# Optimization experiments

Hardware: AMD Instinct MI355X
Metric: run time of the kernel (lower is better)

## Reference

```python
import jax, jax.numpy as jnp
import numpy as np

B, D, C = 4096, 256, 10
KERNEL_MUL = 2.0
KERNEL_NUM = 5


def setup_inputs() -> dict:
    key = jax.random.key(0)
    k1, k2, k3, k4 = jax.random.split(key, 4)
    source = jax.random.normal(k1, (B, D), dtype=jnp.float32)
    target = jax.random.normal(k2, (B, D), dtype=jnp.float32)
    # source_label is consumed as a one-hot matrix by the module
    src_ids = jax.random.randint(k3, (B,), 0, C)
    source_label = jax.nn.one_hot(src_ids, C, dtype=jnp.float32)
    target_logits = jax.random.uniform(k4, (B, C), dtype=jnp.float32)
    return {"source": source, "target": target,
            "source_label": source_label, "target_logits": target_logits}


def _gaussian_kernel(x, y, kernel_mul, kernel_num):
    total = jnp.concatenate([x, y], axis=0)          # [n, d]
    n = total.shape[0]
    sq = jnp.sum(total * total, axis=1)               # [n]
    # ||a-b||^2 = ||a||^2 + ||b||^2 - 2 a.b  (same math, no [n,n,d] tensor)
    l2 = jnp.maximum(sq[:, None] + sq[None, :] - 2.0 * (total @ total.T), 0.0)
    n_f = jnp.asarray(n, l2.dtype)
    bandwidth = jnp.sum(l2) / (n_f * n_f - n_f)
    bandwidth = bandwidth / (kernel_mul ** (kernel_num // 2))
    kernels = jnp.zeros_like(l2)
    for i in range(kernel_num):
        kernels = kernels + jnp.exp(-l2 / (bandwidth * (kernel_mul ** i)))
    return kernels


def _cal_weight(source_label, target_logits, num_class):
    # normalize source one-hot per class column
    s_sum = jnp.sum(source_label, axis=0, keepdims=True)
    s_sum = jnp.where(s_sum == 0, 100.0, s_sum)
    s = source_label / s_sum                           # [Bs, C]
    # hard target labels for presence mask
    t_label = jnp.argmax(target_logits, axis=1)
    t_onehot = jax.nn.one_hot(t_label, num_class, dtype=target_logits.dtype)
    # normalize soft target logits per class column
    t_sum = jnp.sum(target_logits, axis=0, keepdims=True)
    t_sum = jnp.where(t_sum == 0, 100.0, t_sum)
    t = target_logits / t_sum                          # [Bt, C]
    # class is counted only if present in both domains
    mask = (jnp.sum(s, axis=0) > 0) & (jnp.sum(t_onehot, axis=0) > 0)  # [C]
    maskf = mask.astype(s.dtype)
    sm = s * maskf[None, :]
    tm = t * maskf[None, :]
    count = jnp.sum(maskf)
    weight_ss = sm @ sm.T
    weight_tt = tm @ tm.T
    weight_st = sm @ tm.T
    safe = jnp.where(count > 0, count, 1.0)
    weight_ss = jnp.where(count > 0, weight_ss / safe, 0.0)
    weight_tt = jnp.where(count > 0, weight_tt / safe, 0.0)
    weight_st = jnp.where(count > 0, weight_st / safe, 0.0)
    return weight_ss, weight_tt, weight_st


def reference(source, target, source_label, target_logits):
    num_class = target_logits.shape[1]
    bs = source.shape[0]
    w_ss, w_tt, w_st = _cal_weight(source_label, target_logits, num_class)
    kernels = _gaussian_kernel(source, target, KERNEL_MUL, KERNEL_NUM)
    SS = kernels[:bs, :bs]
    TT = kernels[bs:, bs:]
    ST = kernels[:bs, bs:]
    loss = (jnp.sum(w_ss * SS) + jnp.sum(w_tt * TT)
            - 2.0 * jnp.sum(w_st * ST))
    # eval mode: lambda schedule multiplier = 1.0
    return loss * 1.0
```

## Files before the change

kernel.cpp:

```cpp
#include <hip/hip_runtime.h>
#include <hip/hip_bf16.h>

#define N_TOTAL 8192
#define BROWS   4096
#define DDIM    256
#define NCLS    10
#define NB      64
#define NTRI    (NB*(NB+1)/2)

typedef __attribute__((ext_vector_type(8))) short bf16x8;
typedef __attribute__((ext_vector_type(4))) float f32x4;
typedef __attribute__((ext_vector_type(8))) unsigned short u16x8;

static constexpr size_t OFF_X    = 0;
static constexpr size_t OFF_SQ   = 0x400000;
static constexpr size_t OFF_XU   = 0x408000;
static constexpr size_t OFF_CP   = 0x488000;
static constexpr size_t OFF_CLS  = 0x498000;
static constexpr size_t OFF_PRES = 0x499000;
static constexpr size_t OFF_SC   = 0x49A000;
static constexpr size_t OFF_PART = 0x49B000;


__device__ __forceinline__ void gload_lds16(const void* g, void* l) {
    __builtin_amdgcn_global_load_lds((const __attribute__((address_space(1))) void*)g,
                                     (__attribute__((address_space(3))) void*)l, 16, 0, 0);
}

__global__ void k_prep(const float* __restrict__ src, const float* __restrict__ tgt,
                       unsigned short* __restrict__ X, float* __restrict__ sq) {
    int wid  = threadIdx.x >> 6;
    int lane = threadIdx.x & 63;
    int row  = blockIdx.x * 4 + wid;
    const float* p = (row < BROWS) ? (src + (size_t)row * DDIM)
                                   : (tgt + (size_t)(row - BROWS) * DDIM);
    f32x4 v = *reinterpret_cast<const f32x4*>(p + lane * 4);
    unsigned short h[4];
    float ssum = 0.f;
#pragma unroll
    for (int e = 0; e < 4; ++e) {
        unsigned bits = __float_as_uint(v[e]);
        unsigned r = (bits + 0x7FFFu + ((bits >> 16) & 1u)) >> 16;
        h[e] = (unsigned short)r;
        float f = __uint_as_float(r << 16);
        ssum += f * f;
    }
    ushort4 us; us.x = h[0]; us.y = h[1]; us.z = h[2]; us.w = h[3];
    *reinterpret_cast<ushort4*>(X + (size_t)row * DDIM + lane * 4) = us;
#pragma unroll
    for (int off = 32; off > 0; off >>= 1) ssum += __shfl_xor(ssum, off);
    if (lane == 0) sq[row] = ssum;
}

__global__ void k_aux(const unsigned short* __restrict__ X,
                      const float* __restrict__ label, const float* __restrict__ logits,
                      float* __restrict__ colpart, float* __restrict__ clspart,
                      unsigned* __restrict__ prespart) {
    __shared__ float shbuf[8][256];
    __shared__ float cbuf[256][NCLS];
    __shared__ unsigned pm[128];
    int t = threadIdx.x;
    if (blockIdx.x < 64) {
        int b  = blockIdx.x;
        int cg = t & 31;
        int rs = t >> 5;
        const unsigned short* base = X + (size_t)(b * 128 + rs) * DDIM + cg * 8;
        float a[8];
#pragma unroll
        for (int e = 0; e < 8; ++e) a[e] = 0.f;
        for (int i = 0; i < 16; ++i) {
            u16x8 v = *reinterpret_cast<const u16x8*>(base + (size_t)i * 8 * DDIM);
#pragma unroll
            for (int e = 0; e < 8; ++e) a[e] += __uint_as_float((unsigned)v[e] << 16);
        }
#pragma unroll
        for (int e = 0; e < 8; ++e) shbuf[rs][cg * 8 + e] = a[e];
        __syncthreads();
        float s = 0.f;
#pragma unroll
        for (int k = 0; k < 8; ++k) s += shbuf[k][t];
        colpart[b * DDIM + t] = s;
    } else {
        int b = blockIdx.x - 64;
        int r = b * 128 + (t & 127);
        if (t < 128) {
            const float* lr = label + (size_t)r * NCLS;
#pragma unroll
            for (int c = 0; c < NCLS; ++c) cbuf[t][c] = lr[c];
        } else {
            const float* gr = logits + (size_t)r * NCLS;
            float bv = -1e30f; int bc = 0;
#pragma unroll
            for (int c = 0; c < NCLS; ++c) {
                float v = gr[c];
                cbuf[t][c] = v;
                if (v > bv) { bv = v; bc = c; }
            }
            pm[t - 128] = 1u << bc;
        }
        __syncthreads();
        if (t < NCLS) {
            float a = 0.f;
            for (int i = 0; i < 128; ++i) a += cbuf[i][t];
            clspart[b * 20 + t] = a;
        } else if (t < 2 * NCLS) {
            float a = 0.f;
            for (int i = 128; i < 256; ++i) a += cbuf[i][t - NCLS];
            clspart[b * 20 + t] = a;
        }
        if (t == 0) {
            unsigned p = 0;
            for (int i = 0; i < 128; ++i) p |= pm[i];
            prespart[b] = p;
        }
    }
}

__global__ void k_stats(const float* __restrict__ sq, const float* __restrict__ colpart,
                        const float* __restrict__ clspart, const unsigned* __restrict__ prespart,
                        float* __restrict__ scal) {
    __shared__ double dred[256];
    __shared__ float  cfin[2 * NCLS];
    __shared__ unsigned presAll;
    int t = threadIdx.x;

    double cd = 0.0;
    for (int b = 0; b < 64; ++b) cd += (double)colpart[b * DDIM + t];
    dred[t] = cd * cd;
    __syncthreads();
    for (int s = 128; s > 0; s >>= 1) { if (t < s) dred[t] += dred[t + s]; __syncthreads(); }
    double S_cs = dred[0];
    __syncthreads();

    double ss = 0.0;
    for (int k = 0; k < 32; ++k) ss += (double)sq[t + 256 * k];
    dred[t] = ss;
    __syncthreads();
    for (int s = 128; s > 0; s >>= 1) { if (t < s) dred[t] += dred[t + s]; __syncthreads(); }
    double S_sq = dred[0];
    __syncthreads();

    if (t < 2 * NCLS) {
        float a = 0.f;
        for (int b = 0; b < 32; ++b) a += clspart[b * 20 + t];
        cfin[t] = a;
    }
    if (t == 0) {
        unsigned p = 0;
        for (int b = 0; b < 32; ++b) p |= prespart[b];
        presAll = p;
    }
    __syncthreads();

    if (t == 0) {
        double nf = (double)N_TOTAL;
        double sum_l2 = 2.0 * nf * S_sq - 2.0 * S_cs;
        if (sum_l2 < 0.0) sum_l2 = 0.0;
        double bw = sum_l2 / (nf * nf - nf) / 4.0;
        scal[0] = (float)(-1.0 / (16.0 * bw));
        int count = 0;
        for (int c = 0; c < NCLS; ++c) {
            float sv = cfin[c], tv = cfin[NCLS + c];
            bool m = (sv > 0.f) && ((presAll >> c) & 1u);
            count += m ? 1 : 0;
            float sdiv = (sv == 0.f) ? 100.f : sv;
            float tdiv = (tv == 0.f) ? 100.f : tv;
            scal[6  + c] = m ? (1.f / sdiv) : 0.f;
            scal[16 + c] = m ? (1.f / tdiv) : 0.f;
        }
        scal[5] = (float)(count > 0 ? count : 1);
    }
}

__global__ void k_build_xu(const float* __restrict__ label, const float* __restrict__ logits,
                           const float* __restrict__ scal, unsigned short* __restrict__ XU) {
    int r = blockIdx.x * blockDim.x + threadIdx.x;
    if (r >= N_TOTAL) return;
    float v[NCLS];
    if (r < BROWS) {
        const float* lr = label + (size_t)r * NCLS;
#pragma unroll
        for (int c = 0; c < NCLS; ++c) v[c] = lr[c] * scal[6 + c];
    } else {
        const float* gr = logits + (size_t)(r - BROWS) * NCLS;
#pragma unroll
        for (int c = 0; c < NCLS; ++c) v[c] = -gr[c] * scal[16 + c];
    }
    unsigned packed[16];
#pragma unroll
    for (int w = 0; w < 16; ++w) {
        unsigned lo = 0, hi = 0;
        if (2 * w < NCLS) {
            unsigned bits = __float_as_uint(v[2 * w]);
            lo = (bits + 0x7FFFu + ((bits >> 16) & 1u)) >> 16;
        }
        if (2 * w + 1 < NCLS) {
            unsigned bits = __float_as_uint(v[2 * w + 1]);
            hi = (bits + 0x7FFFu + ((bits >> 16) & 1u)) >> 16;
        }
        packed[w] = lo | (hi << 16);
    }
    uint4* out = reinterpret_cast<uint4*>(XU + (size_t)r * 32);
#pragma unroll
    for (int q = 0; q < 4; ++q)
        out[q] = make_uint4(packed[4*q], packed[4*q+1], packed[4*q+2], packed[4*q+3]);
}

__global__ __launch_bounds__(256, 4) void k_main(const unsigned short* __restrict__ X,
                                                 const unsigned short* __restrict__ XU,
                                                 const float* __restrict__ sq,
                                                 const float* __restrict__ scal,
                                                 double* __restrict__ partials) {
    int bid = (blockIdx.x & 7) * (NTRI / 8) + (blockIdx.x >> 3);
    int bi = 0, rem = bid;
    while (rem >= NB - bi) { rem -= NB - bi; ++bi; }
    int bj = bi + rem;

    int tid = threadIdx.x, lane = tid & 63, wid = tid >> 6;
    int wr = wid >> 1, wc = wid & 1;
    int lrow = lane & 15, kgrp = lane >> 4;

    __shared__ unsigned short Abuf[128 * 64];
    __shared__ unsigned short Bbuf[128 * 64];
    __shared__ float red[4];
    char* AbufB = (char*)Abuf;
    char* BbufB = (char*)Bbuf;

    float nb = scal[0];

    f32x4 acc[4][4];
#pragma unroll
    for (int a = 0; a < 4; ++a)
#pragma unroll
        for (int b = 0; b < 4; ++b) acc[a][b] = (f32x4){0.f, 0.f, 0.f, 0.f};

    const size_t arow0 = (size_t)bi * 128;
    const size_t brow0 = (size_t)bj * 128;
    int qthr = wid * 64 + lane;
    int ldsw = wid * 64;

    for (int ks = 0; ks < 4; ++ks) {
#pragma unroll
        for (int it = 0; it < 4; ++it) {
            int q = it * 256 + qthr;
            int r = q >> 3, c = q & 7;
            int cs = c ^ (r & 7);
            size_t goff = (size_t)r * DDIM + ks * 64 + cs * 8;
            size_t loff = (size_t)(it * 256 + ldsw) * 16;
            gload_lds16(X + (arow0 * DDIM + goff), AbufB + loff);
            gload_lds16(X + (brow0 * DDIM + goff), BbufB + loff);
        }
        __syncthreads();

#pragma unroll
        for (int s = 0; s < 2; ++s) {
            int slot = ((s * 4 + kgrp) ^ (lrow & 7)) * 16;
            bf16x8 af[4], bf[4];
#pragma unroll
            for (int f = 0; f < 4; ++f) {
                int ar = wr * 64 + f * 16 + lrow;
                af[f] = *reinterpret_cast<const bf16x8*>(AbufB + ar * 128 + slot);
                int br = wc * 64 + f * 16 + lrow;
                bf[f] = *reinterpret_cast<const bf16x8*>(BbufB + br * 128 + slot);
            }
#pragma unroll
            for (int a = 0; a < 4; ++a)
#pragma unroll
                for (int b = 0; b < 4; ++b)
                    acc[a][b] = __builtin_amdgcn_mfma_f32_16x16x32_bf16(af[a], bf[b], acc[a][b], 0, 0, 0);
        }
        __syncthreads();
    }

    int i0 = bi * 128 + wr * 64;
    int j0 = bj * 128 + wc * 64;
    const unsigned short* AU = XU + (size_t)(i0 + lrow) * 32 + kgrp * 8;
    const unsigned short* BU = XU + (size_t)(j0 + lrow) * 32 + kgrp * 8;
    bf16x8 au[4];
#pragma unroll
    for (int f = 0; f < 4; ++f)
        au[f] = *reinterpret_cast<const bf16x8*>(AU + (size_t)f * 16 * 32);

    float lp = 0.f;
#pragma unroll
    for (int g = 0; g < 4; ++g) {
        bf16x8 bu = *reinterpret_cast<const bf16x8*>(BU + (size_t)g * 16 * 32);
        f32x4 wg[4];
#pragma unroll
        for (int f = 0; f < 4; ++f)
            wg[f] = __builtin_amdgcn_mfma_f32_16x16x32_bf16(au[f], bu, (f32x4){0.f,0.f,0.f,0.f}, 0, 0, 0);

        float sqj = sq[j0 + g * 16 + lrow];
#pragma unroll
        for (int f = 0; f < 4; ++f) {
            f32x4 sqi = *reinterpret_cast<const f32x4*>(sq + i0 + f * 16 + kgrp * 4);
#pragma unroll
            for (int r = 0; r < 4; ++r) {
                float l2 = fmaxf(sqi[r] + sqj - 2.f * acc[f][g][r], 0.f);
                float e1 = __expf(l2 * nb);
                float e2 = e1 * e1;
                float e4 = e2 * e2;
                float e8 = e4 * e4;
                float e16 = e8 * e8;
                float ksum = ((e1 + e2) + (e4 + e8)) + e16;
                lp = fmaf(wg[f][r], ksum, lp);
            }
        }
    }

#pragma unroll
    for (int off = 32; off > 0; off >>= 1) lp += __shfl_xor(lp, off);
    if (lane == 0) red[wid] = lp;
    __syncthreads();
    if (tid == 0)
        partials[bid] = (double)((red[0] + red[1]) + (red[2] + red[3])) * ((bi == bj) ? 1.0 : 2.0);
}

__global__ void k_final(const double* __restrict__ partials, const float* __restrict__ scal,
                        float* __restrict__ out) {
    __shared__ double dred[256];
    int t = threadIdx.x;
    double s = 0.0;
    for (int k = 0; k < 9; ++k) {
        int idx = t + 256 * k;
        if (idx < NTRI) s += partials[idx];
    }
    dred[t] = s;
    __syncthreads();
    for (int st = 128; st > 0; st >>= 1) { if (t < st) dred[t] += dred[t + st]; __syncthreads(); }
    if (t == 0) out[0] = (float)(dred[0] / (double)scal[5]);
}

extern "C" void kernel_launch(void* const* d_in, const int* in_sizes, int n_in,
                              void* d_out, int out_size, void* d_ws, size_t ws_size,
                              hipStream_t stream) {
    const float* src    = (const float*)d_in[0];
    const float* tgt    = (const float*)d_in[1];
    const float* label  = (const float*)d_in[2];
    const float* logits = (const float*)d_in[3];

    char* ws = (char*)d_ws;
    unsigned short* X   = (unsigned short*)(ws + OFF_X);
    float* sq           = (float*)(ws + OFF_SQ);
    unsigned short* XU  = (unsigned short*)(ws + OFF_XU);
    float* colpart      = (float*)(ws + OFF_CP);
    float* clspart      = (float*)(ws + OFF_CLS);
    unsigned* prespart  = (unsigned*)(ws + OFF_PRES);
    float* scal         = (float*)(ws + OFF_SC);
    double* partials    = (double*)(ws + OFF_PART);

    k_prep    <<<2048, 256, 0, stream>>>(src, tgt, X, sq);
    k_aux     <<<96,   256, 0, stream>>>(X, label, logits, colpart, clspart, prespart);
    k_stats   <<<1,    256, 0, stream>>>(sq, colpart, clspart, prespart, scal);
    k_build_xu<<<32,   256, 0, stream>>>(label, logits, scal, XU);
    k_main    <<<NTRI, 256, 0, stream>>>(X, XU, sq, scal, partials);
    k_final   <<<1,    256, 0, stream>>>(partials, scal, (float*)d_out);
}
```

Measured before the change: 64.97 us.

## Fuse prep kernels and double-buffer the K loop in the main Gram kernel

Merges the prep and aux kernels into one launch, with the column sums now read straight from fp32 inputs rounded to bf16, and merges the stats and XU build into one 33-block kernel. This cuts the launch count from six to four. The main kernel switches to a double-buffered LDS pipeline with 32-wide K steps, so the next tile loads while the current one computes, and launch bounds drop to 3 blocks per SM. The epilogue preloads weights and squared norms, folds the bandwidth scale into the norms, and pairs the exp math in 2-wide vectors. More K steps and lower occupancy could offset the gains.

```diff
diff --git a/kernel.cpp b/kernel.cpp
--- a/kernel.cpp
+++ b/kernel.cpp
@@ -7,10 +7,11 @@
 #define NCLS    10
 #define NB      64
 #define NTRI    (NB*(NB+1)/2)
+#define K_STEPS 8
 
 typedef __attribute__((ext_vector_type(8))) short bf16x8;
 typedef __attribute__((ext_vector_type(4))) float f32x4;
-typedef __attribute__((ext_vector_type(8))) unsigned short u16x8;
+typedef __attribute__((ext_vector_type(2))) float f32x2;
 
 static constexpr size_t OFF_X    = 0;
 static constexpr size_t OFF_SQ   = 0x400000;
@@ -26,52 +27,63 @@
     __builtin_amdgcn_global_load_lds((const __attribute__((address_space(1))) void*)g,
                                      (__attribute__((address_space(3))) void*)l, 16, 0, 0);
 }
-
-__global__ void k_prep(const float* __restrict__ src, const float* __restrict__ tgt,
-                       unsigned short* __restrict__ X, float* __restrict__ sq) {
-    int wid  = threadIdx.x >> 6;
-    int lane = threadIdx.x & 63;
-    int row  = blockIdx.x * 4 + wid;
-    const float* p = (row < BROWS) ? (src + (size_t)row * DDIM)
-                                   : (tgt + (size_t)(row - BROWS) * DDIM);
-    f32x4 v = *reinterpret_cast<const f32x4*>(p + lane * 4);
-    unsigned short h[4];
-    float ssum = 0.f;
-#pragma unroll
-    for (int e = 0; e < 4; ++e) {
-        unsigned bits = __float_as_uint(v[e]);
-        unsigned r = (bits + 0x7FFFu + ((bits >> 16) & 1u)) >> 16;
-        h[e] = (unsigned short)r;
-        float f = __uint_as_float(r << 16);
-        ssum += f * f;
-    }
-    ushort4 us; us.x = h[0]; us.y = h[1]; us.z = h[2]; us.w = h[3];
-    *reinterpret_cast<ushort4*>(X + (size_t)row * DDIM + lane * 4) = us;
-#pragma unroll
-    for (int off = 32; off > 0; off >>= 1) ssum += __shfl_xor(ssum, off);
-    if (lane == 0) sq[row] = ssum;
-}
-
-__global__ void k_aux(const unsigned short* __restrict__ X,
+__device__ __forceinline__ float rne_bf16_val(float x) {
+    unsigned b = __float_as_uint(x);
+    unsigned r = (b + 0x7FFFu + ((b >> 16) & 1u)) >> 16;
+    return __uint_as_float(r << 16);
+}
+
+__global__ void k_pre(const float* __restrict__ src, const float* __restrict__ tgt,
                       const float* __restrict__ label, const float* __restrict__ logits,
+                      unsigned short* __restrict__ X, float* __restrict__ sq,
                       float* __restrict__ colpart, float* __restrict__ clspart,
                       unsigned* __restrict__ prespart) {
     __shared__ float shbuf[8][256];
     __shared__ float cbuf[256][NCLS];
     __shared__ unsigned pm[128];
     int t = threadIdx.x;
-    if (blockIdx.x < 64) {
-        int b  = blockIdx.x;
+    int bid = blockIdx.x;
+
+    if (bid < 2048) {
+        int wid  = t >> 6;
+        int lane = t & 63;
+        int row  = bid * 4 + wid;
+        const float* p = (row < BROWS) ? (src + (size_t)row * DDIM)
+                                       : (tgt + (size_t)(row - BROWS) * DDIM);
+        f32x4 v = *reinterpret_cast<const f32x4*>(p + lane * 4);
+        unsigned short h[4];
+        float ssum = 0.f;
+#pragma unroll
+        for (int e = 0; e < 4; ++e) {
+            unsigned bits = __float_as_uint(v[e]);
+            unsigned r = (bits + 0x7FFFu + ((bits >> 16) & 1u)) >> 16;
+            h[e] = (unsigned short)r;
+            float f = __uint_as_float(r << 16);
+            ssum += f * f;
+        }
+        ushort4 us; us.x = h[0]; us.y = h[1]; us.z = h[2]; us.w = h[3];
+        *reinterpret_cast<ushort4*>(X + (size_t)row * DDIM + lane * 4) = us;
+#pragma unroll
+        for (int off = 32; off > 0; off >>= 1) ssum += __shfl_xor(ssum, off);
+        if (lane == 0) sq[row] = ssum;
+    } else if (bid < 2112) {
+        int b  = bid - 2048;
         int cg = t & 31;
         int rs = t >> 5;
-        const unsigned short* base = X + (size_t)(b * 128 + rs) * DDIM + cg * 8;
+        const float* base = (b < 32)
+            ? (src + ((size_t)(b * 128 + rs)) * DDIM + cg * 8)
+            : (tgt + ((size_t)((b - 32) * 128 + rs)) * DDIM + cg * 8);
         float a[8];
 #pragma unroll
         for (int e = 0; e < 8; ++e) a[e] = 0.f;
         for (int i = 0; i < 16; ++i) {
-            u16x8 v = *reinterpret_cast<const u16x8*>(base + (size_t)i * 8 * DDIM);
-#pragma unroll
-            for (int e = 0; e < 8; ++e) a[e] += __uint_as_float((unsigned)v[e] << 16);
+            const float* rp = base + (size_t)i * 8 * DDIM;
+            f32x4 v0 = *reinterpret_cast<const f32x4*>(rp);
+            f32x4 v1 = *reinterpret_cast<const f32x4*>(rp + 4);
+#pragma unroll
+            for (int e = 0; e < 4; ++e) a[e]     += rne_bf16_val(v0[e]);
+#pragma unroll
+            for (int e = 0; e < 4; ++e) a[4 + e] += rne_bf16_val(v1[e]);
         }
 #pragma unroll
         for (int e = 0; e < 8; ++e) shbuf[rs][cg * 8 + e] = a[e];
@@ -81,7 +93,7 @@
         for (int k = 0; k < 8; ++k) s += shbuf[k][t];
         colpart[b * DDIM + t] = s;
     } else {
-        int b = blockIdx.x - 64;
+        int b = bid - 2112;
         int r = b * 128 + (t & 127);
         if (t < 128) {
             const float* lr = label + (size_t)r * NCLS;
@@ -116,48 +128,28 @@
     }
 }
 
-__global__ void k_stats(const float* __restrict__ sq, const float* __restrict__ colpart,
-                        const float* __restrict__ clspart, const unsigned* __restrict__ prespart,
-                        float* __restrict__ scal) {
+__global__ void k_scales(const float* __restrict__ clspart, const unsigned* __restrict__ prespart,
+                         const float* __restrict__ colpart, const float* __restrict__ sq,
+                         const float* __restrict__ label, const float* __restrict__ logits,
+                         float* __restrict__ scal, unsigned short* __restrict__ XU) {
+    __shared__ float  cfin[2 * NCLS];
+    __shared__ float  ascale[NCLS], bscale[NCLS];
+    __shared__ unsigned presAll;
     __shared__ double dred[256];
-    __shared__ float  cfin[2 * NCLS];
-    __shared__ unsigned presAll;
-    int t = threadIdx.x;
-
-    double cd = 0.0;
-    for (int b = 0; b < 64; ++b) cd += (double)colpart[b * DDIM + t];
-    dred[t] = cd * cd;
-    __syncthreads();
-    for (int s = 128; s > 0; s >>= 1) { if (t < s) dred[t] += dred[t + s]; __syncthreads(); }
-    double S_cs = dred[0];
-    __syncthreads();
-
-    double ss = 0.0;
-    for (int k = 0; k < 32; ++k) ss += (double)sq[t + 256 * k];
-    dred[t] = ss;
-    __syncthreads();
-    for (int s = 128; s > 0; s >>= 1) { if (t < s) dred[t] += dred[t + s]; __syncthreads(); }
-    double S_sq = dred[0];
-    __syncthreads();
+    int t = threadIdx.x, b = blockIdx.x;
 
     if (t < 2 * NCLS) {
         float a = 0.f;
-        for (int b = 0; b < 32; ++b) a += clspart[b * 20 + t];
+        for (int k = 0; k < 32; ++k) a += clspart[k * 20 + t];
         cfin[t] = a;
     }
     if (t == 0) {
         unsigned p = 0;
-        for (int b = 0; b < 32; ++b) p |= prespart[b];
+        for (int k = 0; k < 32; ++k) p |= prespart[k];
         presAll = p;
     }
     __syncthreads();
-
     if (t == 0) {
-        double nf = (double)N_TOTAL;
-        double sum_l2 = 2.0 * nf * S_sq - 2.0 * S_cs;
-        if (sum_l2 < 0.0) sum_l2 = 0.0;
-        double bw = sum_l2 / (nf * nf - nf) / 4.0;
-        scal[0] = (float)(-1.0 / (16.0 * bw));
         int count = 0;
         for (int c = 0; c < NCLS; ++c) {
             float sv = cfin[c], tv = cfin[NCLS + c];
@@ -165,48 +157,67 @@
             count += m ? 1 : 0;
             float sdiv = (sv == 0.f) ? 100.f : sv;
             float tdiv = (tv == 0.f) ? 100.f : tv;
-            scal[6  + c] = m ? (1.f / sdiv) : 0.f;
-            scal[16 + c] = m ? (1.f / tdiv) : 0.f;
-        }
-        scal[5] = (float)(count > 0 ? count : 1);
-    }
-}
-
-__global__ void k_build_xu(const float* __restrict__ label, const float* __restrict__ logits,
-                           const float* __restrict__ scal, unsigned short* __restrict__ XU) {
-    int r = blockIdx.x * blockDim.x + threadIdx.x;
-    if (r >= N_TOTAL) return;
-    float v[NCLS];
-    if (r < BROWS) {
-        const float* lr = label + (size_t)r * NCLS;
-#pragma unroll
-        for (int c = 0; c < NCLS; ++c) v[c] = lr[c] * scal[6 + c];
+            ascale[c] = m ? (1.f / sdiv) : 0.f;
+            bscale[c] = m ? (1.f / tdiv) : 0.f;
+        }
+        if (b == 32) scal[5] = (float)(count > 0 ? count : 1);
+    }
+    __syncthreads();
+
+    if (b < 32) {
+        int r = b * 256 + t;
+        float v[NCLS];
+        if (r < BROWS) {
+            const float* lr = label + (size_t)r * NCLS;
+#pragma unroll
+            for (int c = 0; c < NCLS; ++c) v[c] = lr[c] * ascale[c];
+        } else {
+            const float* gr = logits + (size_t)(r - BROWS) * NCLS;
+#pragma unroll
+            for (int c = 0; c < NCLS; ++c) v[c] = -gr[c] * bscale[c];
+        }
+        unsigned packed[16];
+#pragma unroll
+        for (int w = 0; w < 16; ++w) {
+            unsigned lo = 0, hi = 0;
+            if (2 * w < NCLS) {
+                unsigned bits = __float_as_uint(v[2 * w]);
+                lo = (bits + 0x7FFFu + ((bits >> 16) & 1u)) >> 16;
+            }
+            if (2 * w + 1 < NCLS) {
+                unsigned bits = __float_as_uint(v[2 * w + 1]);
+                hi = (bits + 0x7FFFu + ((bits >> 16) & 1u)) >> 16;
+            }
+            packed[w] = lo | (hi << 16);
+        }
+        uint4* out = reinterpret_cast<uint4*>(XU + (size_t)r * 32);
+#pragma unroll
+        for (int q = 0; q < 4; ++q)
+            out[q] = make_uint4(packed[4*q], packed[4*q+1], packed[4*q+2], packed[4*q+3]);
     } else {
-        const float* gr = logits + (size_t)(r - BROWS) * NCLS;
-#pragma unroll
-        for (int c = 0; c < NCLS; ++c) v[c] = -gr[c] * scal[16 + c];
-    }
-    unsigned packed[16];
-#pragma unroll
-    for (int w = 0; w < 16; ++w) {
-        unsigned lo = 0, hi = 0;
-        if (2 * w < NCLS) {
-            unsigned bits = __float_as_uint(v[2 * w]);
-            lo = (bits + 0x7FFFu + ((bits >> 16) & 1u)) >> 16;
-        }
-        if (2 * w + 1 < NCLS) {
-            unsigned bits = __float_as_uint(v[2 * w + 1]);
-            hi = (bits + 0x7FFFu + ((bits >> 16) & 1u)) >> 16;
-        }
-        packed[w] = lo | (hi << 16);
-    }
-    uint4* out = reinterpret_cast<uint4*>(XU + (size_t)r * 32);
-#pragma unroll
-    for (int q = 0; q < 4; ++q)
-        out[q] = make_uint4(packed[4*q], packed[4*q+1], packed[4*q+2], packed[4*q+3]);
-}
-
-__global__ __launch_bounds__(256, 4) void k_main(const unsigned short* __restrict__ X,
+        double cd = 0.0;
+        for (int k = 0; k < 64; ++k) cd += (double)colpart[k * DDIM + t];
+        dred[t] = cd * cd;
+        __syncthreads();
+        for (int s = 128; s > 0; s >>= 1) { if (t < s) dred[t] += dred[t + s]; __syncthreads(); }
+        double S_cs = dred[0];
+        __syncthreads();
+        double ss = 0.0;
+        for (int k = 0; k < 32; ++k) ss += (double)sq[t + 256 * k];
+        dred[t] = ss;
+        __syncthreads();
+        for (int s = 128; s > 0; s >>= 1) { if (t < s) dred[t] += dred[t + s]; __syncthreads(); }
+        if (t == 0) {
+            double nf = (double)N_TOTAL;
+            double sum_l2 = 2.0 * nf * dred[0] - 2.0 * S_cs;
+            if (sum_l2 < 0.0) sum_l2 = 0.0;
+            double bw = sum_l2 / (nf * nf - nf) / 4.0;
+            scal[0] = (float)(-1.0 / (16.0 * bw));
+        }
+    }
+}
+
+__global__ __launch_bounds__(256, 3) void k_main(const unsigned short* __restrict__ X,
                                                  const unsigned short* __restrict__ XU,
                                                  const float* __restrict__ sq,
                                                  const float* __restrict__ scal,
@@ -220,11 +231,11 @@
     int wr = wid >> 1, wc = wid & 1;
     int lrow = lane & 15, kgrp = lane >> 4;
 
-    __shared__ unsigned short Abuf[128 * 64];
-    __shared__ unsigned short Bbuf[128 * 64];
+    __shared__ unsigned short Abuf[2 * 128 * 32];
+    __shared__ unsigned short Bbuf[2 * 128 * 32];
     __shared__ float red[4];
-    char* AbufB = (char*)Abuf;
-    char* BbufB = (char*)Bbuf;
+    char* AB = (char*)Abuf;
+    char* BB = (char*)Bbuf;
 
     float nb = scal[0];
 
@@ -234,41 +245,41 @@
 #pragma unroll
         for (int b = 0; b < 4; ++b) acc[a][b] = (f32x4){0.f, 0.f, 0.f, 0.f};
 
-    const size_t arow0 = (size_t)bi * 128;
-    const size_t brow0 = (size_t)bj * 128;
-    int qthr = wid * 64 + lane;
-    int ldsw = wid * 64;
-
-    for (int ks = 0; ks < 4; ++ks) {
-#pragma unroll
-        for (int it = 0; it < 4; ++it) {
-            int q = it * 256 + qthr;
-            int r = q >> 3, c = q & 7;
-            int cs = c ^ (r & 7);
-            size_t goff = (size_t)r * DDIM + ks * 64 + cs * 8;
-            size_t loff = (size_t)(it * 256 + ldsw) * 16;
-            gload_lds16(X + (arow0 * DDIM + goff), AbufB + loff);
-            gload_lds16(X + (brow0 * DDIM + goff), BbufB + loff);
-        }
-        __syncthreads();
-
-#pragma unroll
-        for (int s = 0; s < 2; ++s) {
-            int slot = ((s * 4 + kgrp) ^ (lrow & 7)) * 16;
-            bf16x8 af[4], bf[4];
-#pragma unroll
-            for (int f = 0; f < 4; ++f) {
-                int ar = wr * 64 + f * 16 + lrow;
-                af[f] = *reinterpret_cast<const bf16x8*>(AbufB + ar * 128 + slot);
-                int br = wc * 64 + f * 16 + lrow;
-                bf[f] = *reinterpret_cast<const bf16x8*>(BbufB + br * 128 + slot);
-            }
-#pragma unroll
-            for (int a = 0; a < 4; ++a)
-#pragma unroll
-                for (int b = 0; b < 4; ++b)
-                    acc[a][b] = __builtin_amdgcn_mfma_f32_16x16x32_bf16(af[a], bf[b], acc[a][b], 0, 0, 0);
-        }
+    const unsigned short* gA0 = X + ((size_t)bi * 128 + (tid >> 2)) * DDIM + (tid & 3) * 8;
+    const unsigned short* gA1 = gA0 + (size_t)64 * DDIM;
+    const unsigned short* gB0 = X + ((size_t)bj * 128 + (tid >> 2)) * DDIM + (tid & 3) * 8;
+    const unsigned short* gB1 = gB0 + (size_t)64 * DDIM;
+    int lds0 = tid * 16;
+    int aoff = (wr * 64 + lrow) * 64 + kgrp * 16;
+    int boff = (wc * 64 + lrow) * 64 + kgrp * 16;
+
+#define STAGE(BS, KS) do { \
+    gload_lds16(gA0 + (KS) * 32, AB + (BS) * 8192 + lds0); \
+    gload_lds16(gA1 + (KS) * 32, AB + (BS) * 8192 + lds0 + 4096); \
+    gload_lds16(gB0 + (KS) * 32, BB + (BS) * 8192 + lds0); \
+    gload_lds16(gB1 + (KS) * 32, BB + (BS) * 8192 + lds0 + 4096); \
+} while (0)
+
+#define COMPUTE(BS) do { \
+    bf16x8 af[4], bf[4]; \
+    _Pragma("unroll") \
+    for (int f = 0; f < 4; ++f) { \
+        af[f] = *reinterpret_cast<const bf16x8*>(AB + (BS) * 8192 + aoff + f * 1024); \
+        bf[f] = *reinterpret_cast<const bf16x8*>(BB + (BS) * 8192 + boff + f * 1024); \
+    } \
+    _Pragma("unroll") \
+    for (int a = 0; a < 4; ++a) \
+        _Pragma("unroll") \
+        for (int b = 0; b < 4; ++b) \
+            acc[a][b] = __builtin_amdgcn_mfma_f32_16x16x32_bf16(af[a], bf[b], acc[a][b], 0, 0, 0); \
+} while (0)
+
+    STAGE(0, 0);
+    __syncthreads();
+#pragma unroll
+    for (int t = 0; t < K_STEPS - 1; ++t) {
+        STAGE((t + 1) & 1, t + 1);
+        COMPUTE(t & 1);
         __syncthreads();
     }
 
@@ -276,37 +287,55 @@
     int j0 = bj * 128 + wc * 64;
     const unsigned short* AU = XU + (size_t)(i0 + lrow) * 32 + kgrp * 8;
     const unsigned short* BU = XU + (size_t)(j0 + lrow) * 32 + kgrp * 8;
-    bf16x8 au[4];
+    bf16x8 au[4], bu[4];
+#pragma unroll
+    for (int f = 0; f < 4; ++f) {
+        au[f] = *reinterpret_cast<const bf16x8*>(AU + (size_t)f * 16 * 32);
+        bu[f] = *reinterpret_cast<const bf16x8*>(BU + (size_t)f * 16 * 32);
+    }
+    f32x4 sqin[4];
 #pragma unroll
     for (int f = 0; f < 4; ++f)
-        au[f] = *reinterpret_cast<const bf16x8*>(AU + (size_t)f * 16 * 32);
-
-    float lp = 0.f;
+        sqin[f] = *reinterpret_cast<const f32x4*>(sq + i0 + f * 16 + kgrp * 4);
+    float sqjn[4];
+#pragma unroll
+    for (int g = 0; g < 4; ++g) sqjn[g] = sq[j0 + g * 16 + lrow];
+
+    COMPUTE((K_STEPS - 1) & 1);
+
+#pragma unroll
+    for (int f = 0; f < 4; ++f) sqin[f] *= nb;
+#pragma unroll
+    for (int g = 0; g < 4; ++g) sqjn[g] *= nb;
+    float m2nb = -2.f * nb;
+
+    f32x2 lp2 = (f32x2){0.f, 0.f};
 #pragma unroll
     for (int g = 0; g < 4; ++g) {
-        bf16x8 bu = *reinterpret_cast<const bf16x8*>(BU + (size_t)g * 16 * 32);
-        f32x4 wg[4];
+        f32x4 wf[4];
 #pragma unroll
         for (int f = 0; f < 4; ++f)
-            wg[f] = __builtin_amdgcn_mfma_f32_16x16x32_bf16(au[f], bu, (f32x4){0.f,0.f,0.f,0.f}, 0, 0, 0);
-
-        float sqj = sq[j0 + g * 16 + lrow];
+            wf[f] = __builtin_amdgcn_mfma_f32_16x16x32_bf16(au[f], bu[g], (f32x4){0.f,0.f,0.f,0.f}, 0, 0, 0);
 #pragma unroll
         for (int f = 0; f < 4; ++f) {
-            f32x4 sqi = *reinterpret_cast<const f32x4*>(sq + i0 + f * 16 + kgrp * 4);
-#pragma unroll
-            for (int r = 0; r < 4; ++r) {
-                float l2 = fmaxf(sqi[r] + sqj - 2.f * acc[f][g][r], 0.f);
-                float e1 = __expf(l2 * nb);
-                float e2 = e1 * e1;
-                float e4 = e2 * e2;
-                float e8 = e4 * e4;
-                float e16 = e8 * e8;
-                float ksum = ((e1 + e2) + (e4 + e8)) + e16;
-                lp = fmaf(wg[f][r], ksum, lp);
+#pragma unroll
+            for (int h = 0; h < 2; ++h) {
+                f32x2 ssn = (f32x2){ sqin[f][2*h] + sqjn[g], sqin[f][2*h+1] + sqjn[g] };
+                f32x2 tt  = (f32x2){ fmaf(acc[f][g][2*h],   m2nb, ssn.x),
+                                     fmaf(acc[f][g][2*h+1], m2nb, ssn.y) };
+                tt.x = fminf(tt.x, 0.f);
+                tt.y = fminf(tt.y, 0.f);
+                f32x2 e;
+                e.x = __expf(tt.x);
+                e.y = __expf(tt.y);
+                f32x2 e2 = e * e, e4 = e2 * e2, e8 = e4 * e4, e16 = e8 * e8;
+                f32x2 ks = ((e + e2) + (e4 + e8)) + e16;
+                lp2.x = fmaf(wf[f][2*h],   ks.x, lp2.x);
+                lp2.y = fmaf(wf[f][2*h+1], ks.y, lp2.y);
             }
         }
     }
+    float lp = lp2.x + lp2.y;
 
 #pragma unroll
     for (int off = 32; off > 0; off >>= 1) lp += __shfl_xor(lp, off);
@@ -314,6 +343,8 @@
     __syncthreads();
     if (tid == 0)
         partials[bid] = (double)((red[0] + red[1]) + (red[2] + red[3])) * ((bi == bj) ? 1.0 : 2.0);
+#undef STAGE
+#undef COMPUTE
 }
 
 __global__ void k_final(const double* __restrict__ partials, const float* __restrict__ scal,
@@ -349,10 +380,8 @@
     float* scal         = (float*)(ws + OFF_SC);
     double* partials    = (double*)(ws + OFF_PART);
 
-    k_prep    <<<2048, 256, 0, stream>>>(src, tgt, X, sq);
-    k_aux     <<<96,   256, 0, stream>>>(X, label, logits, colpart, clspart, prespart);
-    k_stats   <<<1,    256, 0, stream>>>(sq, colpart, clspart, prespart, scal);
-    k_build_xu<<<32,   256, 0, stream>>>(label, logits, scal, XU);
-    k_main    <<<NTRI, 256, 0, stream>>>(X, XU, sq, scal, partials);
-    k_final   <<<1,    256, 0, stream>>>(partials, scal, (float*)d_out);
-}
+    k_pre    <<<2144, 256, 0, stream>>>(src, tgt, label, logits, X, sq, colpart, clspart, prespart);
+    k_scales <<<33,   256, 0, stream>>>(clspart, prespart, colpart, sq, label, logits, scal, XU);
+    k_main   <<<NTRI, 256, 0, stream>>>(X, XU, sq, scal, partials);
+    k_final  <<<1,    256, 0, stream>>>(partials, scal, (float*)d_out);
+}
```

Measured after the change: 56.45 us, median of 3. -13.1%, faster.
